# Performance work log

Measured on AMD Instinct MI355X. Metric: run time of the kernel, lower is better.

## Reference

```python
import jax, jax.numpy as jnp
import numpy as np

BETA = 0.25  # commitment cost


def setup_inputs() -> dict:
    key = jax.random.key(0)
    k1, k2 = jax.random.split(key)
    B, C, T = 16, 256, 1024      # batch, emb_dim channels, sequence length
    N_EMB = 8192                 # codebook size
    z = jax.random.normal(k1, (B, C, T), dtype=jnp.float32)
    # original init: uniform(-1/n_emb, 1/n_emb); scale a normal similarly small
    emb = jax.random.normal(k2, (N_EMB, C), dtype=jnp.float32) * (1.0 / N_EMB)
    return {"z": z, "emb": emb}


def reference(z, emb):
    sg = jax.lax.stop_gradient
    # [B, C, T] -> [B, T, C]
    zt = jnp.transpose(z, (0, 2, 1))
    B, T, C = zt.shape
    zf = zt.reshape(-1, C)  # [B*T, C]
    # squared euclidean distances: ||z||^2 + ||e||^2 - 2 z.e  -> [B*T, N]
    d = (jnp.sum(zf * zf, axis=1, keepdims=True)
         + jnp.sum(emb * emb, axis=1)
         - 2.0 * jnp.einsum('bd,nd->bn', zf, emb))
    idx = jnp.argmin(d, axis=-1)               # [B*T]
    z_q = emb[idx].reshape(B, T, C)            # [B, T, C]
    loss = (BETA * jnp.mean((sg(z_q) - zt) ** 2)
            + jnp.mean((z_q - sg(zt)) ** 2))
    # straight-through estimator
    z_q = zt + sg(z_q - zt)
    z_q = jnp.transpose(z_q, (0, 2, 1))        # back to [B, C, T]
    return z_q, loss, idx
```

## Files before the change

### kernel.cpp

```cpp
#include <hip/hip_runtime.h>


#define C_    256
#define T_    1024
#define M_    16384
#define N_    8192

#define OUT_ZQ   0
#define OUT_LOSS 4194304
#define OUT_IDX  4194305

#define WS_SZ    0
#define WS_SE    16384
#define WS_PART  24576
#define MIN_OFF  131072u
#define FB_OFF   8519680u
#define WS_NEED  16908288u
#define O_I1     24576
#define O_I2     40960
#define O_PART   73728

typedef __attribute__((ext_vector_type(8))) short bf16x8;
typedef __attribute__((ext_vector_type(4))) float f32x4;
typedef unsigned long long ull;

__device__ __forceinline__ unsigned short f2b(float f) {
    unsigned u = __float_as_uint(f);
    return (unsigned short)((u + 0x7FFFu + ((u >> 16) & 1u)) >> 16);
}
__device__ __forceinline__ float b2f(unsigned short u) {
    return __uint_as_float(((unsigned)u) << 16);
}

__global__ __launch_bounds__(256) void vq_sums(const float* __restrict__ z,
                                               const float* __restrict__ emb,
                                               float* __restrict__ ws) {
    int gid = blockIdx.x * 256 + threadIdx.x;
    if (gid < M_) {
        int b = gid >> 10, t = gid & (T_ - 1);
        const float* zp = z + (size_t)b * C_ * T_ + t;
        float blk[2];
#pragma unroll
        for (int h = 0; h < 2; ++h) {
            float r[8];
#pragma unroll
            for (int j = 0; j < 8; ++j) {
                float v = zp[(size_t)(h * 128 + j) * T_];
                r[j] = __fmul_rn(v, v);
            }
            for (int i = 8; i < 128; i += 8)
#pragma unroll
                for (int j = 0; j < 8; ++j) {
                    float v = zp[(size_t)(h * 128 + i + j) * T_];
                    r[j] = __fadd_rn(r[j], __fmul_rn(v, v));
                }
            blk[h] = __fadd_rn(__fadd_rn(__fadd_rn(r[0], r[1]), __fadd_rn(r[2], r[3])),
                               __fadd_rn(__fadd_rn(r[4], r[5]), __fadd_rn(r[6], r[7])));
        }
        ws[WS_SZ + gid] = __fadd_rn(blk[0], blk[1]);
    } else if (gid < M_ + N_) {
        int n = gid - M_;
        const float* ep = emb + (size_t)n * C_;
        float blk[2];
#pragma unroll
        for (int h = 0; h < 2; ++h) {
            float r[8];
#pragma unroll
            for (int j = 0; j < 8; ++j) {
                float v = ep[h * 128 + j];
                r[j] = __fmul_rn(v, v);
            }
            for (int i = 8; i < 128; i += 8)
#pragma unroll
                for (int j = 0; j < 8; ++j) {
                    float v = ep[h * 128 + i + j];
                    r[j] = __fadd_rn(r[j], __fmul_rn(v, v));
                }
            blk[h] = __fadd_rn(__fadd_rn(__fadd_rn(r[0], r[1]), __fadd_rn(r[2], r[3])),
                               __fadd_rn(__fadd_rn(r[4], r[5]), __fadd_rn(r[6], r[7])));
        }
        ws[WS_SE + n] = __fadd_rn(blk[0], blk[1]);
    }
}

__global__ __launch_bounds__(256) void vq_prep_b(const float* __restrict__ emb,
                                                 char* __restrict__ fb) {
    int gid = blockIdx.x * 256 + threadIdx.x;
    int n = gid >> 5, kg = gid & 31;
    const float* ep = emb + (size_t)n * C_ + kg * 8;
    unsigned hi[8], lo[8];
#pragma unroll
    for (int j = 0; j < 8; ++j) {
        float v = ep[j];
        unsigned short h = f2b(v);
        hi[j] = h;
        lo[j] = f2b(v - b2f(h));
    }
    int nt = n >> 4, kt = kg >> 2, lane = (kg & 3) * 16 + (n & 15);
    size_t base = ((size_t)((nt * 8 + kt) * 2) << 10) + (lane << 4);
    uint4 hv = {hi[0] | (hi[1] << 16), hi[2] | (hi[3] << 16), hi[4] | (hi[5] << 16), hi[6] | (hi[7] << 16)};
    uint4 lv = {lo[0] | (lo[1] << 16), lo[2] | (lo[3] << 16), lo[4] | (lo[5] << 16), lo[6] | (lo[7] << 16)};
    *(uint4*)(fb + base) = hv;
    *(uint4*)(fb + base + 1024) = lv;
}

__global__ __launch_bounds__(256, 1) void vq_mfma4(
        const float* __restrict__ z, const char* __restrict__ fb,
        const float* __restrict__ sz, const float* __restrict__ se,
        ull* __restrict__ minima) {
    __shared__ __align__(16) char ldsA[65536];
    __shared__ __align__(16) char ldsB[65536];

    const int tid = threadIdx.x;
    const int lane = tid & 63;
    const int w = tid >> 6;
    const int quad = lane >> 4, li = lane & 15;
    const int mb = blockIdx.x, ns = blockIdx.y;
    const int ns256 = ns << 8;

#define STAGEB(nt_, kt_, buf_) do {                                                   \
    _Pragma("unroll")                                                                 \
    for (int i_ = 0; i_ < 8; ++i_) {                                                  \
        int f_ = (w << 3) + i_;                                                       \
        int ntb_ = f_ >> 1, pp_ = f_ & 1;                                             \
        size_t goff_ = ((size_t)((((ns256 + ((nt_) << 4) + ntb_) << 3) + (kt_)) * 2 + pp_) << 10) + (lane << 4); \
        __builtin_amdgcn_global_load_lds(                                             \
            (__attribute__((address_space(1))) unsigned*)(size_t)(fb + goff_),        \
            (__attribute__((address_space(3))) unsigned*)(unsigned)(size_t)(ldsB + ((buf_) << 15) + (f_ << 10)), \
            16, 0, 0);                                                                \
    }                                                                                 \
} while (0)

    STAGEB(0, 0, 0);

    {
        const float* zb = z + (size_t)(mb >> 4) * C_ * T_ + ((mb & 15) << 6);
#pragma unroll
        for (int p = 0; p < 4; ++p) {
            int c  = p * 64 + (tid >> 2);
            int tq = tid & 3;
            const float* src = zb + (size_t)c * T_ + tq * 16;
            int kt = c >> 5, kg3 = (c >> 3) & 3, j = c & 7;
            unsigned short* d0 = (unsigned short*)(ldsA + (((tq * 8 + kt) * 2 + 0) << 10) + (kg3 << 8) + (j << 1));
            unsigned short* d1 = (unsigned short*)(ldsA + (((tq * 8 + kt) * 2 + 1) << 10) + (kg3 << 8) + (j << 1));
#pragma unroll
            for (int u = 0; u < 4; ++u) {
                float4 v = *(const float4*)(src + u * 4);
                float vv[4] = {v.x, v.y, v.z, v.w};
#pragma unroll
                for (int e = 0; e < 4; ++e) {
                    unsigned short h = f2b(vv[e]);
                    unsigned short l = f2b(vv[e] - b2f(h));
                    int i = u * 4 + e;
                    d0[i * 8] = h;
                    d1[i * 8] = l;
                }
            }
        }
    }
    __syncthreads();

    float szr[16];
#pragma unroll
    for (int mt = 0; mt < 4; ++mt)
#pragma unroll
        for (int r = 0; r < 4; ++r)
            szr[mt * 4 + r] = sz[(mb << 6) + (mt << 4) + (quad << 2) + r];

    ull key[16];
#pragma unroll
    for (int s = 0; s < 16; ++s) key[s] = ~0ULL;

    for (int nt = 0; nt < 16; ++nt) {
        f32x4 acc[4][4];
#pragma unroll
        for (int i = 0; i < 4; ++i)
#pragma unroll
            for (int j = 0; j < 4; ++j) acc[i][j] = (f32x4){0.f, 0.f, 0.f, 0.f};

#pragma unroll
        for (int kt = 0; kt < 8; ++kt) {
            if (kt < 7)       STAGEB(nt, kt + 1, (kt + 1) & 1);
            else if (nt < 15) STAGEB(nt + 1, 0, 0);

            const char* bB = ldsB + ((kt & 1) << 15);
            bf16x8 ah[4], al[4];
#pragma unroll
            for (int mt = 0; mt < 4; ++mt) {
                ah[mt] = *(const bf16x8*)(ldsA + ((((mt << 3) + kt) * 2 + 0) << 10) + (lane << 4));
                al[mt] = *(const bf16x8*)(ldsA + ((((mt << 3) + kt) * 2 + 1) << 10) + (lane << 4));
            }
#pragma unroll
            for (int nt4 = 0; nt4 < 4; ++nt4) {
                const char* bp = bB + ((((w << 2) + nt4) * 2) << 10) + (lane << 4);
                bf16x8 bh = *(const bf16x8*)(bp);
                bf16x8 bl = *(const bf16x8*)(bp + 1024);
#pragma unroll
                for (int mt = 0; mt < 4; ++mt) {
                    f32x4 c = acc[mt][nt4];
                    c = __builtin_amdgcn_mfma_f32_16x16x32_bf16(ah[mt], bh, c, 0, 0, 0);
                    c = __builtin_amdgcn_mfma_f32_16x16x32_bf16(ah[mt], bl, c, 0, 0, 0);
                    c = __builtin_amdgcn_mfma_f32_16x16x32_bf16(al[mt], bh, c, 0, 0, 0);
                    acc[mt][nt4] = c;
                }
            }

            if (kt == 7) {
                float sev[4];
#pragma unroll
                for (int nt4 = 0; nt4 < 4; ++nt4)
                    sev[nt4] = se[(ns << 12) + (nt << 8) + (((w << 2) + nt4) << 4) + li];
#pragma unroll
                for (int mt = 0; mt < 4; ++mt)
#pragma unroll
                    for (int r = 0; r < 4; ++r) {
                        int sl = (mt << 2) + r;
                        ull best = key[sl];
#pragma unroll
                        for (int nt4 = 0; nt4 < 4; ++nt4) {
                            int ncol = (ns << 12) + (nt << 8) + (((w << 2) + nt4) << 4) + li;
                            float s = fmaf(-2.f, acc[mt][nt4][r], __fadd_rn(szr[sl], sev[nt4]));
                            ull k = ((ull)__float_as_uint(s) << 32) | (unsigned)ncol;
                            if (k < best) best = k;
                        }
                        key[sl] = best;
                    }
                if (nt & 1) {
#pragma unroll
                    for (int sl = 0; sl < 16; ++sl) {
                        ull kk = key[sl];
#pragma unroll
                        for (int off = 1; off <= 8; off <<= 1) {
                            ull o = __shfl_xor(kk, off, 64);
                            if (o < kk) kk = o;
                        }
                        if (li == 0) {
                            int row = (mb << 6) + ((sl >> 2) << 4) + (quad << 2) + (sl & 3);
                            minima[(size_t)row * 64 + (ns << 5) + ((nt >> 1) << 2) + w] = kk;
                        }
                        key[sl] = ~0ULL;
                    }
                }
            }
            __syncthreads();
        }
    }
#undef STAGEB
}

__global__ __launch_bounds__(256) void vq_pick2(
        const float* __restrict__ z, const float* __restrict__ emb,
        const float* __restrict__ ws, const ull* __restrict__ minima,
        float* __restrict__ out) {
    __shared__ float Lz[256 * 17];
    const float* sz = ws + WS_SZ;
    const float* se = ws + WS_SE;
    const int tid = threadIdx.x;
    const int w = tid >> 6, lane = tid & 63, li = lane & 15;
    const int m0 = blockIdx.x * 16;
    const int b = m0 >> 10, t0 = m0 & (T_ - 1);

    {
        const float* src = z + (size_t)b * C_ * T_ + (size_t)tid * T_ + t0;
#pragma unroll
        for (int u = 0; u < 4; ++u) {
            float4 v = *(const float4*)(src + u * 4);
            Lz[tid * 17 + u * 4 + 0] = v.x;
            Lz[tid * 17 + u * 4 + 1] = v.y;
            Lz[tid * 17 + u * 4 + 2] = v.z;
            Lz[tid * 17 + u * 4 + 3] = v.w;
        }
    }
    __syncthreads();

    for (int rr = 0; rr < 4; ++rr) {
        const int tloc = w * 4 + rr;
        const int m = m0 + tloc;
        ull kmin = minima[(size_t)m * 64 + lane];
        int cand[4];
#pragma unroll
        for (int rep = 0; rep < 4; ++rep) {
            ull bf = kmin;
#pragma unroll
            for (int off = 1; off <= 32; off <<= 1) {
                ull o = __shfl_xor(bf, off, 64);
                if (o < bf) bf = o;
            }
            int ix = (int)(unsigned)(bf & 0xFFFFFFFFull);
            cand[rep] = ix < 0 ? 0 : (ix > N_ - 1 ? N_ - 1 : ix);
            if (kmin == bf) kmin = ~0ULL;
        }
        const int cn = cand[lane >> 4];
        const float* ep = emb + (size_t)cn * C_;
        double sum = 0.0;
#pragma unroll
        for (int cc = 0; cc < 16; ++cc) {
            int c = cc * 16 + li;
            sum = fma((double)Lz[c * 17 + tloc], (double)ep[c], sum);
        }
#pragma unroll
        for (int off = 1; off <= 8; off <<= 1)
            sum += __shfl_xor(sum, off, 64);
        double s0 = __shfl(sum, 0, 64), s1 = __shfl(sum, 16, 64);
        double s2 = __shfl(sum, 32, 64), s3 = __shfl(sum, 48, 64);
        if (lane == 0) {
            float szm = sz[m];
            float d0 = fmaf(-2.f, (float)s0, __fadd_rn(szm, se[cand[0]]));
            float d1 = fmaf(-2.f, (float)s1, __fadd_rn(szm, se[cand[1]]));
            float d2 = fmaf(-2.f, (float)s2, __fadd_rn(szm, se[cand[2]]));
            float d3 = fmaf(-2.f, (float)s3, __fadd_rn(szm, se[cand[3]]));
            float bd = d0; int bi = cand[0];
            if (d1 < bd || (d1 == bd && cand[1] < bi)) { bd = d1; bi = cand[1]; }
            if (d2 < bd || (d2 == bd && cand[2] < bi)) { bd = d2; bi = cand[2]; }
            if (d3 < bd || (d3 == bd && cand[3] < bi)) { bd = d3; bi = cand[3]; }
            out[OUT_IDX + m] = (float)bi;
        }
    }
}

__global__ __launch_bounds__(256) void vq_pass1_fp32(
        const float* __restrict__ z,
        const float* __restrict__ emb,
        float* __restrict__ ws) {
    __shared__ float As[32][68];
    __shared__ float Bs[32][68];
    const float* s_z = ws + WS_SZ;
    const float* s_e = ws + WS_SE;
    int* i1ws = (int*)ws + O_I1;
    int* i2ws = (int*)ws + O_I2;
    const int tid = threadIdx.x;
    const int mt  = blockIdx.x;
    const int tx  = tid & 15, ty = tid >> 4;
    const int b   = mt >> 4;
    const int t0  = (mt << 6) & (T_ - 1);
    const float* zbase = z + (size_t)b * C_ * T_ + t0;
    const int a_k = tid >> 4;
    const int a_m = (tid & 15) << 2;
    const int b_j = tid >> 2;
    const int b_q = (tid & 3) << 3;
    const float4 sz4 = *(const float4*)(s_z + mt * 64 + (ty << 2));
    const float szv[4] = {sz4.x, sz4.y, sz4.z, sz4.w};
    float v1[4], v2[4];
    int   i1[4], i2[4];
#pragma unroll
    for (int i = 0; i < 4; ++i) {
        v1[i] = INFINITY; v2[i] = INFINITY;
        i1[i] = 0x7FFFFFFF; i2[i] = 0x7FFFFFFF;
    }
    for (int nt = 0; nt < N_ / 64; ++nt) {
        const int n0 = nt * 64;
        float acc[4][4];
#pragma unroll
        for (int i = 0; i < 4; ++i)
#pragma unroll
            for (int j = 0; j < 4; ++j) acc[i][j] = 0.f;
        for (int kt = 0; kt < C_; kt += 32) {
            __syncthreads();
#pragma unroll
            for (int p = 0; p < 2; ++p) {
                int k = a_k + p * 16;
                float4 af = *(const float4*)(zbase + (size_t)(kt + k) * T_ + a_m);
                *(float4*)&As[k][a_m] = af;
            }
            {
                const float* ep = emb + (size_t)(n0 + b_j) * C_ + kt + b_q;
                float4 e0 = ((const float4*)ep)[0];
                float4 e1 = ((const float4*)ep)[1];
                Bs[b_q + 0][b_j] = e0.x; Bs[b_q + 1][b_j] = e0.y;
                Bs[b_q + 2][b_j] = e0.z; Bs[b_q + 3][b_j] = e0.w;
                Bs[b_q + 4][b_j] = e1.x; Bs[b_q + 5][b_j] = e1.y;
                Bs[b_q + 6][b_j] = e1.z; Bs[b_q + 7][b_j] = e1.w;
            }
            __syncthreads();
#pragma unroll
            for (int k = 0; k < 32; ++k) {
                const float4 a  = *(const float4*)&As[k][ty << 2];
                const float4 bv = *(const float4*)&Bs[k][tx << 2];
                acc[0][0] = fmaf(a.x, bv.x, acc[0][0]);
                acc[0][1] = fmaf(a.x, bv.y, acc[0][1]);
                acc[0][2] = fmaf(a.x, bv.z, acc[0][2]);
                acc[0][3] = fmaf(a.x, bv.w, acc[0][3]);
                acc[1][0] = fmaf(a.y, bv.x, acc[1][0]);
                acc[1][1] = fmaf(a.y, bv.y, acc[1][1]);
                acc[1][2] = fmaf(a.y, bv.z, acc[1][2]);
                acc[1][3] = fmaf(a.y, bv.w, acc[1][3]);
                acc[2][0] = fmaf(a.z, bv.x, acc[2][0]);
                acc[2][1] = fmaf(a.z, bv.y, acc[2][1]);
                acc[2][2] = fmaf(a.z, bv.z, acc[2][2]);
                acc[2][3] = fmaf(a.z, bv.w, acc[2][3]);
                acc[3][0] = fmaf(a.w, bv.x, acc[3][0]);
                acc[3][1] = fmaf(a.w, bv.y, acc[3][1]);
                acc[3][2] = fmaf(a.w, bv.z, acc[3][2]);
                acc[3][3] = fmaf(a.w, bv.w, acc[3][3]);
            }
        }
        const float4 se4 = *(const float4*)(s_e + n0 + (tx << 2));
        const float sev[4] = {se4.x, se4.y, se4.z, se4.w};
#pragma unroll
        for (int j = 0; j < 4; ++j) {
            const int n = n0 + (tx << 2) + j;
#pragma unroll
            for (int i = 0; i < 4; ++i) {
                float A = __fadd_rn(szv[i], sev[j]);
                float s = fmaf(-2.f, acc[i][j], A);
                if (s < v1[i]) { v2[i] = v1[i]; i2[i] = i1[i]; v1[i] = s; i1[i] = n; }
                else if (s < v2[i]) { v2[i] = s; i2[i] = n; }
            }
        }
    }
#pragma unroll
    for (int i = 0; i < 4; ++i) {
        float a1 = v1[i], a2 = v2[i];
        int   y1 = i1[i], y2 = i2[i];
#pragma unroll
        for (int off = 8; off >= 1; off >>= 1) {
            float o1 = __shfl_xor(a1, off, 64); int p1 = __shfl_xor(y1, off, 64);
            float o2 = __shfl_xor(a2, off, 64); int p2 = __shfl_xor(y2, off, 64);
            bool alt = (o1 < a1) || (o1 == a1 && p1 < y1);
            float w1 = alt ? o1 : a1; int q1 = alt ? p1 : y1;
            float lv = alt ? a1 : o1; int lq = alt ? y1 : p1;
            float wv = alt ? o2 : a2; int wq = alt ? p2 : y2;
            bool sb = (lv < wv) || (lv == wv && lq < wq);
            a2 = sb ? lv : wv; y2 = sb ? lq : wq;
            a1 = w1; y1 = q1;
        }
        if (tx == 0) {
            int m = mt * 64 + (ty << 2) + i;
            i1ws[m] = y1;
            i2ws[m] = y2;
        }
    }
}

__global__ __launch_bounds__(256) void vq_pass2_fp32(
        const float* __restrict__ z,
        const float* __restrict__ emb,
        float* __restrict__ ws,
        float* __restrict__ out) {
    const float* s_z = ws + WS_SZ;
    const float* s_e = ws + WS_SE;
    const int* i1ws = (const int*)ws + O_I1;
    const int* i2ws = (const int*)ws + O_I2;
    const int tid  = threadIdx.x;
    const int wave = tid >> 6, lane = tid & 63;
    const int half = lane >> 5;
    const int c0   = (lane & 31) << 3;
    const int rowbase = (blockIdx.x * 4 + wave) * 64;
    for (int r = 0; r < 64; ++r) {
        const int m = rowbase + r;
        int c1 = i1ws[m], c2 = i2ws[m];
        c1 = c1 < 0 ? 0 : (c1 > N_ - 1 ? N_ - 1 : c1);
        c2 = c2 < 0 ? 0 : (c2 > N_ - 1 ? N_ - 1 : c2);
        const int b = m >> 10, t = m & (T_ - 1);
        const float* zp = z + (size_t)b * C_ * T_ + t;
        const int cand = half ? c2 : c1;
        const float* ep = emb + (size_t)cand * C_;
        double sum = 0.0;
#pragma unroll
        for (int c = 0; c < 8; ++c)
            sum = fma((double)zp[(size_t)(c0 + c) * T_], (double)ep[c0 + c], sum);
#pragma unroll
        for (int off = 1; off <= 16; off <<= 1)
            sum += __shfl_xor(sum, off, 64);
        double s1 = __shfl(sum, 0, 64);
        double s2 = __shfl(sum, 32, 64);
        if (lane == 0) {
            float p1 = (float)s1, p2 = (float)s2;
            float d1 = fmaf(-2.f, p1, __fadd_rn(s_z[m], s_e[c1]));
            float d2 = fmaf(-2.f, p2, __fadd_rn(s_z[m], s_e[c2]));
            int win = ((d2 < d1) || (d2 == d1 && c2 < c1)) ? c2 : c1;
            out[OUT_IDX + m] = (float)win;
        }
    }
}

__global__ __launch_bounds__(256) void vq_gather(
        const float* __restrict__ z,
        const float* __restrict__ emb,
        float* __restrict__ partial,
        float* __restrict__ out) {
    __shared__ float Ls[64][129];
    __shared__ int   idxs[64];
    __shared__ float wred[4];
    const int tid = threadIdx.x;
    const int mg  = blockIdx.x;
    const int m0  = mg << 6;
    const int b   = m0 >> 10;
    const int t0  = m0 & (T_ - 1);
    if (tid < 64) {
        int ix = (int)out[OUT_IDX + m0 + tid];
        idxs[tid] = ix < 0 ? 0 : (ix > N_ - 1 ? N_ - 1 : ix);
    }
    __syncthreads();
    float lsum = 0.f;
    const int w = tid >> 6, l = tid & 63;
    const int tt2 = tid & 63, c0 = tid >> 6;
    const size_t base = (size_t)b * (C_ * T_) + t0 + tt2;
#pragma unroll
    for (int ch = 0; ch < 2; ++ch) {
        __syncthreads();
#pragma unroll
        for (int it = 0; it < 8; ++it) {
            int tt = it * 8 + w * 2 + (l >> 5);
            int cq = l & 31;
            int row = idxs[tt];
            float4 ev = *(const float4*)(emb + (size_t)row * C_ + ch * 128 + (cq << 2));
            Ls[tt][(cq << 2) + 0] = ev.x;
            Ls[tt][(cq << 2) + 1] = ev.y;
            Ls[tt][(cq << 2) + 2] = ev.z;
            Ls[tt][(cq << 2) + 3] = ev.w;
        }
        __syncthreads();
#pragma unroll
        for (int st = 0; st < 32; ++st) {
            int c_l = (st << 2) + c0;
            int c   = (ch << 7) + c_l;
            float v = Ls[tt2][c_l];
            size_t off = base + (size_t)c * T_;
            out[OUT_ZQ + off] = v;
            float d = v - z[off];
            lsum = fmaf(d, d, lsum);
        }
    }
#pragma unroll
    for (int off = 32; off >= 1; off >>= 1) lsum += __shfl_xor(lsum, off, 64);
    if (l == 0) wred[w] = lsum;
    __syncthreads();
    if (tid == 0) partial[mg] = wred[0] + wred[1] + wred[2] + wred[3];
}

__global__ __launch_bounds__(256) void vq_loss(const float* __restrict__ partial,
                                               float* __restrict__ out) {
    __shared__ float wred[4];
    const int tid = threadIdx.x;
    float v = partial[tid];
#pragma unroll
    for (int off = 32; off >= 1; off >>= 1) v += __shfl_xor(v, off, 64);
    if ((tid & 63) == 0) wred[tid >> 6] = v;
    __syncthreads();
    if (tid == 0)
        out[OUT_LOSS] = (wred[0] + wred[1] + wred[2] + wred[3]) * (1.25f / 4194304.f);
}

extern "C" void kernel_launch(void* const* d_in, const int* in_sizes, int n_in,
                              void* d_out, int out_size, void* d_ws, size_t ws_size,
                              hipStream_t stream) {
    const float* z   = (const float*)d_in[0];
    const float* emb = (const float*)d_in[1];
    float* out = (float*)d_out;
    float* ws  = (float*)d_ws;

    vq_sums<<<dim3((M_ + N_) / 256), dim3(256), 0, stream>>>(z, emb, ws);

    if (ws_size >= WS_NEED) {
        char* fb = (char*)d_ws + FB_OFF;
        ull* minima = (ull*)((char*)d_ws + MIN_OFF);
        vq_prep_b<<<dim3(1024), dim3(256), 0, stream>>>(emb, fb);
        vq_mfma4<<<dim3(256, 2), dim3(256), 0, stream>>>(z, fb, ws + WS_SZ, ws + WS_SE, minima);
        vq_pick2<<<dim3(1024), dim3(256), 0, stream>>>(z, emb, ws, minima, out);
        vq_gather<<<dim3(M_ / 64), dim3(256), 0, stream>>>(z, emb, ws + WS_PART, out);
        vq_loss<<<dim3(1), dim3(256), 0, stream>>>(ws + WS_PART, out);
    } else {
        vq_pass1_fp32<<<dim3(M_ / 64), dim3(256), 0, stream>>>(z, emb, ws);
        vq_pass2_fp32<<<dim3(64), dim3(256), 0, stream>>>(z, emb, ws, out);
        vq_gather<<<dim3(M_ / 64), dim3(256), 0, stream>>>(z, emb, ws + O_PART, out);
        vq_loss<<<dim3(1), dim3(256), 0, stream>>>(ws + O_PART, out);
    }
}
```

Measured before the change: 354.7 us.

## Give each wave private B staging and drop block barriers in MFMA kernel

The distance-MFMA kernel now uses one block per 64-row tile that covers the whole codebook, where before two blocks each covered half. Each wave stages its own slice of codebook tiles into a private double-buffered LDS region and synchronises with s_waitcnt instead of __syncthreads. The A operand (z hi/lo) is held in registers for the whole kernel rather than reloaded from LDS each k-step. This removes the block-wide barriers and the repeated A reads, at the cost of much higher register pressure and only 256 blocks, which may underfill the CUs.

```diff
diff --git a/kernel.cpp b/kernel.cpp
--- a/kernel.cpp
+++ b/kernel.cpp
@@ -104,7 +104,7 @@
     *(uint4*)(fb + base + 1024) = lv;
 }
 
-__global__ __launch_bounds__(256, 1) void vq_mfma4(
+__global__ __launch_bounds__(256, 1) void vq_mfma5(
         const float* __restrict__ z, const char* __restrict__ fb,
         const float* __restrict__ sz, const float* __restrict__ se,
         ull* __restrict__ minima) {
@@ -115,23 +115,25 @@
     const int lane = tid & 63;
     const int w = tid >> 6;
     const int quad = lane >> 4, li = lane & 15;
-    const int mb = blockIdx.x, ns = blockIdx.y;
-    const int ns256 = ns << 8;
-
-#define STAGEB(nt_, kt_, buf_) do {                                                   \
+    const int mb = blockIdx.x;
+
+    char* wbuf = ldsB + (w << 14);
+
+#define NTILE0(nt_) ((((nt_) >> 1) << 5) + (w << 3) + (((nt_) & 1) << 2))
+
+#define STAGEB(ntile0_, kt_, buf_) do {                                               \
     _Pragma("unroll")                                                                 \
-    for (int i_ = 0; i_ < 8; ++i_) {                                                  \
-        int f_ = (w << 3) + i_;                                                       \
+    for (int f_ = 0; f_ < 8; ++f_) {                                                  \
         int ntb_ = f_ >> 1, pp_ = f_ & 1;                                             \
-        size_t goff_ = ((size_t)((((ns256 + ((nt_) << 4) + ntb_) << 3) + (kt_)) * 2 + pp_) << 10) + (lane << 4); \
+        size_t goff_ = ((size_t)((((ntile0_) + ntb_) * 8 + (kt_)) * 2 + pp_) << 10) + (lane << 4); \
         __builtin_amdgcn_global_load_lds(                                             \
             (__attribute__((address_space(1))) unsigned*)(size_t)(fb + goff_),        \
-            (__attribute__((address_space(3))) unsigned*)(unsigned)(size_t)(ldsB + ((buf_) << 15) + (f_ << 10)), \
+            (__attribute__((address_space(3))) unsigned*)(unsigned)(size_t)(wbuf + ((buf_) << 13) + (f_ << 10)), \
             16, 0, 0);                                                                \
     }                                                                                 \
 } while (0)
 
-    STAGEB(0, 0, 0);
+    STAGEB(NTILE0(0), 0, 0);
 
     {
         const float* zb = z + (size_t)(mb >> 4) * C_ * T_ + ((mb & 15) << 6);
@@ -160,6 +162,15 @@
     }
     __syncthreads();
 
+    bf16x8 Ah[4][8], Al[4][8];
+#pragma unroll
+    for (int mt = 0; mt < 4; ++mt)
+#pragma unroll
+        for (int kt = 0; kt < 8; ++kt) {
+            Ah[mt][kt] = *(const bf16x8*)(ldsA + ((((mt << 3) + kt) * 2 + 0) << 10) + (lane << 4));
+            Al[mt][kt] = *(const bf16x8*)(ldsA + ((((mt << 3) + kt) * 2 + 1) << 10) + (lane << 4));
+        }
+
     float szr[16];
 #pragma unroll
     for (int mt = 0; mt < 4; ++mt)
@@ -171,7 +182,8 @@
 #pragma unroll
     for (int s = 0; s < 16; ++s) key[s] = ~0ULL;
 
-    for (int nt = 0; nt < 16; ++nt) {
+    for (int nt = 0; nt < 32; ++nt) {
+        const int ntile0 = NTILE0(nt);
         f32x4 acc[4][4];
 #pragma unroll
         for (int i = 0; i < 4; ++i)
@@ -180,72 +192,70 @@
 
 #pragma unroll
         for (int kt = 0; kt < 8; ++kt) {
-            if (kt < 7)       STAGEB(nt, kt + 1, (kt + 1) & 1);
-            else if (nt < 15) STAGEB(nt + 1, 0, 0);
-
-            const char* bB = ldsB + ((kt & 1) << 15);
-            bf16x8 ah[4], al[4];
-#pragma unroll
-            for (int mt = 0; mt < 4; ++mt) {
-                ah[mt] = *(const bf16x8*)(ldsA + ((((mt << 3) + kt) * 2 + 0) << 10) + (lane << 4));
-                al[mt] = *(const bf16x8*)(ldsA + ((((mt << 3) + kt) * 2 + 1) << 10) + (lane << 4));
-            }
+            const int cb = kt & 1;
+            if (kt < 7)       STAGEB(ntile0, kt + 1, cb ^ 1);
+            else if (nt < 31) STAGEB(NTILE0(nt + 1), 0, cb ^ 1);
+            if (kt == 7 && nt == 31) {
+                asm volatile("s_waitcnt vmcnt(0)" ::: "memory");
+            } else {
+                asm volatile("s_waitcnt vmcnt(8)" ::: "memory");
+            }
+            __builtin_amdgcn_sched_barrier(0);
 #pragma unroll
             for (int nt4 = 0; nt4 < 4; ++nt4) {
-                const char* bp = bB + ((((w << 2) + nt4) * 2) << 10) + (lane << 4);
+                const char* bp = wbuf + (cb << 13) + ((nt4 * 2) << 10) + (lane << 4);
                 bf16x8 bh = *(const bf16x8*)(bp);
                 bf16x8 bl = *(const bf16x8*)(bp + 1024);
 #pragma unroll
                 for (int mt = 0; mt < 4; ++mt) {
                     f32x4 c = acc[mt][nt4];
-                    c = __builtin_amdgcn_mfma_f32_16x16x32_bf16(ah[mt], bh, c, 0, 0, 0);
-                    c = __builtin_amdgcn_mfma_f32_16x16x32_bf16(ah[mt], bl, c, 0, 0, 0);
-                    c = __builtin_amdgcn_mfma_f32_16x16x32_bf16(al[mt], bh, c, 0, 0, 0);
+                    c = __builtin_amdgcn_mfma_f32_16x16x32_bf16(Ah[mt][kt], bh, c, 0, 0, 0);
+                    c = __builtin_amdgcn_mfma_f32_16x16x32_bf16(Ah[mt][kt], bl, c, 0, 0, 0);
+                    c = __builtin_amdgcn_mfma_f32_16x16x32_bf16(Al[mt][kt], bh, c, 0, 0, 0);
                     acc[mt][nt4] = c;
                 }
             }
-
-            if (kt == 7) {
-                float sev[4];
-#pragma unroll
-                for (int nt4 = 0; nt4 < 4; ++nt4)
-                    sev[nt4] = se[(ns << 12) + (nt << 8) + (((w << 2) + nt4) << 4) + li];
-#pragma unroll
-                for (int mt = 0; mt < 4; ++mt)
-#pragma unroll
-                    for (int r = 0; r < 4; ++r) {
-                        int sl = (mt << 2) + r;
-                        ull best = key[sl];
-#pragma unroll
-                        for (int nt4 = 0; nt4 < 4; ++nt4) {
-                            int ncol = (ns << 12) + (nt << 8) + (((w << 2) + nt4) << 4) + li;
-                            float s = fmaf(-2.f, acc[mt][nt4][r], __fadd_rn(szr[sl], sev[nt4]));
-                            ull k = ((ull)__float_as_uint(s) << 32) | (unsigned)ncol;
-                            if (k < best) best = k;
-                        }
-                        key[sl] = best;
-                    }
-                if (nt & 1) {
-#pragma unroll
-                    for (int sl = 0; sl < 16; ++sl) {
-                        ull kk = key[sl];
-#pragma unroll
-                        for (int off = 1; off <= 8; off <<= 1) {
-                            ull o = __shfl_xor(kk, off, 64);
-                            if (o < kk) kk = o;
-                        }
-                        if (li == 0) {
-                            int row = (mb << 6) + ((sl >> 2) << 4) + (quad << 2) + (sl & 3);
-                            minima[(size_t)row * 64 + (ns << 5) + ((nt >> 1) << 2) + w] = kk;
-                        }
-                        key[sl] = ~0ULL;
-                    }
-                }
-            }
-            __syncthreads();
+            __builtin_amdgcn_sched_barrier(0);
+        }
+
+        float sev[4];
+#pragma unroll
+        for (int nt4 = 0; nt4 < 4; ++nt4)
+            sev[nt4] = se[((ntile0 + nt4) << 4) + li];
+#pragma unroll
+        for (int mt = 0; mt < 4; ++mt)
+#pragma unroll
+            for (int r = 0; r < 4; ++r) {
+                int sl = (mt << 2) + r;
+                ull best = key[sl];
+#pragma unroll
+                for (int nt4 = 0; nt4 < 4; ++nt4) {
+                    int ncol = ((ntile0 + nt4) << 4) + li;
+                    float s = fmaf(-2.f, acc[mt][nt4][r], __fadd_rn(szr[sl], sev[nt4]));
+                    ull k = ((ull)__float_as_uint(s) << 32) | (unsigned)ncol;
+                    if (k < best) best = k;
+                }
+                key[sl] = best;
+            }
+        if (nt & 1) {
+#pragma unroll
+            for (int sl = 0; sl < 16; ++sl) {
+                ull kk = key[sl];
+#pragma unroll
+                for (int off = 1; off <= 8; off <<= 1) {
+                    ull o = __shfl_xor(kk, off, 64);
+                    if (o < kk) kk = o;
+                }
+                if (li == 0) {
+                    int row = (mb << 6) + ((sl >> 2) << 4) + (quad << 2) + (sl & 3);
+                    minima[(size_t)row * 64 + (((nt >> 1) << 2) + w)] = kk;
+                }
+                key[sl] = ~0ULL;
+            }
         }
     }
 #undef STAGEB
+#undef NTILE0
 }
 
 __global__ __launch_bounds__(256) void vq_pick2(
@@ -556,7 +566,7 @@
         char* fb = (char*)d_ws + FB_OFF;
         ull* minima = (ull*)((char*)d_ws + MIN_OFF);
         vq_prep_b<<<dim3(1024), dim3(256), 0, stream>>>(emb, fb);
-        vq_mfma4<<<dim3(256, 2), dim3(256), 0, stream>>>(z, fb, ws + WS_SZ, ws + WS_SE, minima);
+        vq_mfma5<<<dim3(256), dim3(256), 0, stream>>>(z, fb, ws + WS_SZ, ws + WS_SE, minima);
         vq_pick2<<<dim3(1024), dim3(256), 0, stream>>>(z, emb, ws, minima, out);
         vq_gather<<<dim3(M_ / 64), dim3(256), 0, stream>>>(z, emb, ws + WS_PART, out);
         vq_loss<<<dim3(1), dim3(256), 0, stream>>>(ws + WS_PART, out);
```

After: 349.0 us, median of 2. About the same (-1.6%).
